# Performance work log

Hardware: AMD Instinct MI355X
Metric: run time of the kernel (lower is better)

## Reference

```python
import jax, jax.numpy as jnp
import numpy as np

N_NODES, N_FEAT, N_HID, N_CLS = 50000, 128, 64, 16
N_EDGES, N_EDGES2 = 800000, 3000000


def _rand_edges(key, n_edges, n_nodes):
    # self-loop-free random edge list [2, E] (src, dst)
    k1, k2 = jax.random.split(key)
    src = jax.random.randint(k1, (n_edges,), 0, n_nodes)
    off = jax.random.randint(k2, (n_edges,), 1, n_nodes)
    dst = (src + off) % n_nodes
    return jnp.stack([src, dst]).astype(jnp.int64)


def setup_inputs() -> dict:
    key = jax.random.key(0)
    ks = jax.random.split(key, 8)
    x = jax.random.normal(ks[0], (N_NODES, N_FEAT), jnp.float32)
    edge_index = _rand_edges(ks[1], N_EDGES, N_NODES)    # original edges, no self loops
    edge_index2 = _rand_edges(ks[2], N_EDGES2, N_NODES)  # exclusive 2-hop edges
    w1 = jax.random.normal(ks[3], (N_FEAT, N_HID), jnp.float32) / np.sqrt(N_FEAT)
    b1 = jnp.zeros((N_HID,), jnp.float32)
    w2 = jax.random.normal(ks[4], (3 * N_HID, N_CLS), jnp.float32) / np.sqrt(3 * N_HID)
    b2 = jnp.zeros((N_CLS,), jnp.float32)
    lin_w = jax.random.normal(ks[5], (3 * N_CLS, N_CLS), jnp.float32) / np.sqrt(3 * N_CLS)
    lin_b = jnp.zeros((N_CLS,), jnp.float32)
    return {"x": x, "w1": w1, "b1": b1, "w2": w2, "b2": b2,
            "lin_w": lin_w, "lin_b": lin_b,
            "edge_index": edge_index, "edge_index2": edge_index2}


def _gcn_conv(h, W, b, ei, n):
    # PyG GCNConv(add_self_loops=False): transform, symmetric-normalize, scatter-add, bias.
    hw = h @ W                                   # [n, d_out]
    src, dst = ei[0], ei[1]
    ones = jnp.ones(ei.shape[1], h.dtype)
    deg = jax.ops.segment_sum(ones, dst, num_segments=n)       # in-degree
    dinv = jnp.where(deg > 0, jax.lax.rsqrt(jnp.maximum(deg, 1e-12)), 0.0)
    norm = dinv[src] * dinv[dst]                 # [E]
    msg = hw[src] * norm[:, None]                # gather + scale (traffic-bound)
    return jax.ops.segment_sum(msg, dst, num_segments=n) + b


def reference(x, w1, b1, w2, b2, lin_w, lin_b, edge_index, edge_index2):
    n = x.shape[0]
    # layer 1: three branches over (original edges, 2-hop edges, self-loop-only)
    h1 = _gcn_conv(x, w1, b1, edge_index, n)
    h1_2 = _gcn_conv(x, w1, b1, edge_index2, n)
    h1_3 = x @ w1 + b1                           # self-loop-only GCN: deg=1, norm=1
    R1 = jax.nn.relu(jnp.concatenate([h1, h1_2, h1_3], axis=1))  # dropout = identity (eval)
    # layer 2: same three branches with shared gcn2 weights
    h2 = _gcn_conv(R1, w2, b2, edge_index, n)
    h2_2 = _gcn_conv(R1, w2, b2, edge_index2, n)
    h2_3 = R1 @ w2 + b2
    R2 = jnp.concatenate([h2, h2_2, h2_3], axis=1)
    out = R2 @ lin_w + lin_b
    return jax.nn.log_softmax(out, axis=1)
```

## Files before the change

### kernel.cpp

```cpp
#include <hip/hip_runtime.h>
#include <math.h>


#define NPB    64
#define CHUNK  16384
#define HCHUNK 16384

typedef unsigned short us8 __attribute__((ext_vector_type(8)));

__device__ inline float b2f(unsigned short u) {
    return __uint_as_float(((unsigned int)u) << 16);
}
__device__ inline unsigned short f2b(float f) {
    unsigned int u = __float_as_uint(f);
    u = (u + 0x7FFFu + ((u >> 16) & 1u)) >> 16;
    return (unsigned short)u;
}

__global__ void __launch_bounds__(256)
k_gemm1(const float* __restrict__ x, const float* __restrict__ w1,
        unsigned short* __restrict__ hwb, int n) {
    __shared__ float ws[128 * 64];
    __shared__ float xs[64 * 128];
    int t = threadIdx.x;
    int row0 = blockIdx.x * 64;
    for (int i = t; i < 128 * 16; i += 256)
        ((float4*)ws)[i] = ((const float4*)w1)[i];
    for (int i = t; i < 64 * 32; i += 256) {
        int r = row0 + (i >> 5);
        ((float4*)xs)[i] = (r < n) ? ((const float4*)x)[r * 32 + (i & 31)]
                                   : make_float4(0.f, 0.f, 0.f, 0.f);
    }
    __syncthreads();
    int tr = t >> 4, tc = t & 15;
    float acc[4][4] = {};
    #pragma unroll 4
    for (int k4 = 0; k4 < 32; ++k4) {
        float4 wv0 = *(const float4*)&ws[(k4 * 4 + 0) * 64 + tc * 4];
        float4 wv1 = *(const float4*)&ws[(k4 * 4 + 1) * 64 + tc * 4];
        float4 wv2 = *(const float4*)&ws[(k4 * 4 + 2) * 64 + tc * 4];
        float4 wv3 = *(const float4*)&ws[(k4 * 4 + 3) * 64 + tc * 4];
        #pragma unroll
        for (int r = 0; r < 4; ++r) {
            float4 xv = *(const float4*)&xs[(tr * 4 + r) * 128 + k4 * 4];
            acc[r][0] = fmaf(xv.x, wv0.x, acc[r][0]);
            acc[r][1] = fmaf(xv.x, wv0.y, acc[r][1]);
            acc[r][2] = fmaf(xv.x, wv0.z, acc[r][2]);
            acc[r][3] = fmaf(xv.x, wv0.w, acc[r][3]);
            acc[r][0] = fmaf(xv.y, wv1.x, acc[r][0]);
            acc[r][1] = fmaf(xv.y, wv1.y, acc[r][1]);
            acc[r][2] = fmaf(xv.y, wv1.z, acc[r][2]);
            acc[r][3] = fmaf(xv.y, wv1.w, acc[r][3]);
            acc[r][0] = fmaf(xv.z, wv2.x, acc[r][0]);
            acc[r][1] = fmaf(xv.z, wv2.y, acc[r][1]);
            acc[r][2] = fmaf(xv.z, wv2.z, acc[r][2]);
            acc[r][3] = fmaf(xv.z, wv2.w, acc[r][3]);
            acc[r][0] = fmaf(xv.w, wv3.x, acc[r][0]);
            acc[r][1] = fmaf(xv.w, wv3.y, acc[r][1]);
            acc[r][2] = fmaf(xv.w, wv3.z, acc[r][2]);
            acc[r][3] = fmaf(xv.w, wv3.w, acc[r][3]);
        }
    }
    #pragma unroll
    for (int r = 0; r < 4; ++r) {
        int rr = row0 + tr * 4 + r;
        if (rr < n) {
            ushort4 o;
            o.x = f2b(acc[r][0]); o.y = f2b(acc[r][1]);
            o.z = f2b(acc[r][2]); o.w = f2b(acc[r][3]);
            *(ushort4*)&hwb[rr * 64 + tc * 4] = o;
        }
    }
}

__global__ void k_hist2(const int* __restrict__ dstA, int* __restrict__ bhA, int EA, int nbA,
                        const int* __restrict__ dstB, int* __restrict__ bhB, int EB) {
    __shared__ int lh[1024];
    const int* dst; int* bh; int E; int cb;
    if ((int)blockIdx.x < nbA) { dst = dstA; bh = bhA; E = EA; cb = blockIdx.x; }
    else                       { dst = dstB; bh = bhB; E = EB; cb = blockIdx.x - nbA; }
    int t = threadIdx.x;
    for (int i = t; i < 1024; i += 256) lh[i] = 0;
    __syncthreads();
    int base = cb * HCHUNK;
    int cnt = min(HCHUNK, E - base);
    for (int i = t; i < cnt; i += 256) atomicAdd(&lh[dst[base + i] >> 6], 1);
    __syncthreads();
    for (int b = t; b < 1024; b += 256)
        if (lh[b]) atomicAdd(&bh[b], lh[b]);
}

__global__ void k_bscan(const int* __restrict__ bhA, int* __restrict__ bbA, int* __restrict__ bcA,
                        const int* __restrict__ bhB, int* __restrict__ bbB, int* __restrict__ bcB,
                        int B) {
    const int* bh = blockIdx.x ? bhB : bhA;
    int* bb = blockIdx.x ? bbB : bbA;
    int* bc = blockIdx.x ? bcB : bcA;
    int t = threadIdx.x;
    int carry = 0;
    int nch = (B + 63) >> 6;
    for (int c = 0; c < nch; ++c) {
        int idx = c * 64 + t;
        int v = (idx < B) ? bh[idx] : 0;
        int incl = v;
        #pragma unroll
        for (int off = 1; off < 64; off <<= 1) {
            int tv = __shfl_up(incl, off);
            if (t >= off) incl += tv;
        }
        if (idx < B) { bb[idx] = incl - v + carry; bc[idx] = incl - v + carry; }
        carry += __shfl(incl, 63);
    }
    if (t == 0) bb[B] = carry;
}

__global__ void __launch_bounds__(1024)
k_part2(const int* __restrict__ srcA, const int* __restrict__ dstA,
        int* __restrict__ bcurA, unsigned int* __restrict__ outA, int EA, int nbA,
        const int* __restrict__ srcB, const int* __restrict__ dstB,
        int* __restrict__ bcurB, unsigned int* __restrict__ outB, int EB) {
    __shared__ int lh[1024];
    __shared__ int loff[1024];
    __shared__ int gof[1024];
    __shared__ int lcur[1024];
    __shared__ unsigned int stage[CHUNK];
    const int *src, *dst; int *bcur; unsigned int *out; int E, cb;
    if ((int)blockIdx.x < nbA) { src = srcA; dst = dstA; bcur = bcurA; out = outA; E = EA; cb = blockIdx.x; }
    else                       { src = srcB; dst = dstB; bcur = bcurB; out = outB; E = EB; cb = blockIdx.x - nbA; }
    int t = threadIdx.x;
    int base = cb * CHUNK;
    int cnt = min(CHUNK, E - base);
    lh[t] = 0;
    __syncthreads();
    for (int i = t; i < cnt; i += 1024) atomicAdd(&lh[dst[base + i] >> 6], 1);
    __syncthreads();
    int vdeg = lh[t];
    int incl = vdeg;
    #pragma unroll
    for (int off = 1; off < 64; off <<= 1) {
        int tv = __shfl_up(incl, off);
        if ((t & 63) >= off) incl += tv;
    }
    if ((t & 63) == 63) gof[t >> 6] = incl;
    __syncthreads();
    if (t < 16) {
        int wv = gof[t];
        int winc = wv;
        #pragma unroll
        for (int off = 1; off < 16; off <<= 1) {
            int tv = __shfl_up(winc, off, 16);
            if (t >= off) winc += tv;
        }
        gof[16 + t] = winc - wv;
    }
    __syncthreads();
    int excl = incl - vdeg + gof[16 + (t >> 6)];
    loff[t] = excl;
    lcur[t] = excl;
    __syncthreads();
    gof[t] = vdeg ? atomicAdd(&bcur[t], vdeg) : 0;
    __syncthreads();
    for (int i = t; i < cnt; i += 1024) {
        int d = dst[base + i];
        int s = src[base + i];
        int bkt = d >> 6;
        int p = atomicAdd(&lcur[bkt], 1);
        stage[p] = (unsigned int)s | ((unsigned int)(d & 63) << 16) |
                   ((unsigned int)bkt << 22);
    }
    __syncthreads();
    for (int i = t; i < cnt; i += 1024) {
        unsigned int e = stage[i];
        int bkt = (int)(e >> 22);
        out[gof[bkt] + (i - loff[bkt])] = e & 0x3FFFFFu;
    }
}

__global__ void __launch_bounds__(256)
k_csr2(const int* __restrict__ bbaseA, const unsigned int* __restrict__ ebufA,
       int* __restrict__ rsA, float* __restrict__ dvA, unsigned short* __restrict__ ssrcA, int EA,
       const int* __restrict__ bbaseB, const unsigned int* __restrict__ ebufB,
       int* __restrict__ rsB, float* __restrict__ dvB, unsigned short* __restrict__ ssrcB, int EB,
       int B, int n) {
    __shared__ int cnt[64];
    __shared__ int lcur[64];
    const int* bbase; const unsigned int* ebuf; int* rs; float* dv;
    unsigned short* ssrc; int b, Etot;
    if ((int)blockIdx.x < B) { bbase = bbaseA; ebuf = ebufA; rs = rsA; dv = dvA; ssrc = ssrcA; b = blockIdx.x; Etot = EA; }
    else                     { bbase = bbaseB; ebuf = ebufB; rs = rsB; dv = dvB; ssrc = ssrcB; b = blockIdx.x - B; Etot = EB; }
    int t = threadIdx.x;
    if (t < 64) cnt[t] = 0;
    __syncthreads();
    int beg = bbase[b], end = bbase[b + 1];
    for (int i = beg + t; i < end; i += 256)
        atomicAdd(&cnt[(ebuf[i] >> 16) & 63u], 1);
    __syncthreads();
    if (t < 64) {
        int v = cnt[t];
        int incl = v;
        #pragma unroll
        for (int off = 1; off < 64; off <<= 1) {
            int tv = __shfl_up(incl, off);
            if (t >= off) incl += tv;
        }
        int start = beg + incl - v;
        lcur[t] = start;
        int node = b * NPB + t;
        if (node < n) {
            rs[node] = start;
            dv[node] = (v > 0) ? rsqrtf((float)v) : 0.f;
        }
    }
    __syncthreads();
    for (int i = beg + t; i < end; i += 256) {
        unsigned int e = ebuf[i];
        int p = atomicAdd(&lcur[(e >> 16) & 63u], 1);
        ssrc[p] = (unsigned short)(e & 0xFFFFu);
    }
    if (t == 0 && b == B - 1) rs[n] = Etot;
}

__global__ void k_pack(const unsigned short* __restrict__ ssrc1, const float* __restrict__ dinv1,
                       unsigned int* __restrict__ p1, int E1,
                       const unsigned short* __restrict__ ssrc2, const float* __restrict__ dinv2,
                       unsigned int* __restrict__ p2, int E2) {
    int stride = gridDim.x * 256;
    for (int i = blockIdx.x * 256 + threadIdx.x; i < E1 + E2; i += stride) {
        if (i < E1) {
            int s = ssrc1[i];
            p1[i] = (unsigned int)s | ((unsigned int)f2b(dinv1[s]) << 16);
        } else {
            int j = i - E1;
            int s = ssrc2[j];
            p2[j] = (unsigned int)s | ((unsigned int)f2b(dinv2[s]) << 16);
        }
    }
}

__device__ inline void agg64_body(const int* __restrict__ rs,
                                  const unsigned int* __restrict__ psrc,
                                  const float* __restrict__ dinv,
                                  const us8* __restrict__ hwb8,
                                  const float* __restrict__ b1,
                                  unsigned short* __restrict__ R1b,
                                  int col_unit, int n, int tid) {
    int v = tid >> 3, q = tid & 7;
    if (v >= n) return;
    int beg = rs[v], end = rs[v + 1];
    float a[8] = {0.f, 0.f, 0.f, 0.f, 0.f, 0.f, 0.f, 0.f};
    int i = beg;
    for (; i + 8 <= end; i += 8) {
        unsigned int e0 = psrc[i + 0], e1 = psrc[i + 1], e2 = psrc[i + 2], e3 = psrc[i + 3];
        unsigned int e4 = psrc[i + 4], e5 = psrc[i + 5], e6 = psrc[i + 6], e7 = psrc[i + 7];
        int s0 = e0 & 0xFFFFu, s1 = e1 & 0xFFFFu, s2 = e2 & 0xFFFFu, s3 = e3 & 0xFFFFu;
        int s4 = e4 & 0xFFFFu, s5 = e5 & 0xFFFFu, s6 = e6 & 0xFFFFu, s7 = e7 & 0xFFFFu;
        float c0 = b2f((unsigned short)(e0 >> 16)), c1 = b2f((unsigned short)(e1 >> 16));
        float c2 = b2f((unsigned short)(e2 >> 16)), c3 = b2f((unsigned short)(e3 >> 16));
        float c4 = b2f((unsigned short)(e4 >> 16)), c5 = b2f((unsigned short)(e5 >> 16));
        float c6 = b2f((unsigned short)(e6 >> 16)), c7 = b2f((unsigned short)(e7 >> 16));
        us8 h0 = hwb8[s0 * 8 + q], h1 = hwb8[s1 * 8 + q];
        us8 h2 = hwb8[s2 * 8 + q], h3 = hwb8[s3 * 8 + q];
        us8 h4 = hwb8[s4 * 8 + q], h5 = hwb8[s5 * 8 + q];
        us8 h6 = hwb8[s6 * 8 + q], h7 = hwb8[s7 * 8 + q];
        #pragma unroll
        for (int j = 0; j < 8; ++j) {
            a[j] = fmaf(b2f(h0[j]), c0, a[j]);
            a[j] = fmaf(b2f(h1[j]), c1, a[j]);
            a[j] = fmaf(b2f(h2[j]), c2, a[j]);
            a[j] = fmaf(b2f(h3[j]), c3, a[j]);
            a[j] = fmaf(b2f(h4[j]), c4, a[j]);
            a[j] = fmaf(b2f(h5[j]), c5, a[j]);
            a[j] = fmaf(b2f(h6[j]), c6, a[j]);
            a[j] = fmaf(b2f(h7[j]), c7, a[j]);
        }
    }
    for (; i < end; ++i) {
        unsigned int e = psrc[i];
        int s = e & 0xFFFFu;
        float sc = b2f((unsigned short)(e >> 16));
        us8 h = hwb8[s * 8 + q];
        #pragma unroll
        for (int j = 0; j < 8; ++j) a[j] = fmaf(b2f(h[j]), sc, a[j]);
    }
    float dd = dinv[v];
    us8 o;
    #pragma unroll
    for (int j = 0; j < 8; ++j) {
        float r = fmaf(a[j], dd, b1[q * 8 + j]);
        o[j] = f2b(r > 0.f ? r : 0.f);
    }
    ((us8*)&R1b[v * 192])[col_unit + q] = o;
}

__global__ void k_agg1f(const int* __restrict__ rs1, const unsigned int* __restrict__ psrc1,
                        const float* __restrict__ dinv1,
                        const int* __restrict__ rs2, const unsigned int* __restrict__ psrc2,
                        const float* __restrict__ dinv2,
                        const us8* __restrict__ hwb8, const float* __restrict__ b1,
                        unsigned short* __restrict__ R1b, int n, int nba) {
    int bid = blockIdx.x;
    if (bid < nba) {
        agg64_body(rs2, psrc2, dinv2, hwb8, b1, R1b, 8, n, bid * 256 + threadIdx.x);
    } else if (bid < 2 * nba) {
        agg64_body(rs1, psrc1, dinv1, hwb8, b1, R1b, 0, n,
                   (bid - nba) * 256 + threadIdx.x);
    } else {
        int tid = (bid - 2 * nba) * 256 + threadIdx.x;
        int v = tid >> 3, q = tid & 7;
        if (v >= n) return;
        us8 h = hwb8[v * 8 + q];
        us8 o;
        #pragma unroll
        for (int j = 0; j < 8; ++j) {
            float r = b2f(h[j]) + b1[q * 8 + j];
            o[j] = f2b(r > 0.f ? r : 0.f);
        }
        ((us8*)&R1b[v * 192])[16 + q] = o;
    }
}

__global__ void __launch_bounds__(256)
k_gemm2(const unsigned short* __restrict__ R1b, const float* __restrict__ w2,
        unsigned short* __restrict__ hwb2, int n) {
    __shared__ float ws[192 * 16];
    __shared__ float rs[16][193];
    int t = threadIdx.x;
    for (int i = t; i < 192 * 16; i += 256) ws[i] = w2[i];
    int row0 = blockIdx.x * 16;
    for (int i = t; i < 16 * 192; i += 256) {
        int r = i / 192, j = i - r * 192;
        int v = row0 + r;
        rs[r][j] = (v < n) ? b2f(R1b[v * 192 + j]) : 0.f;
    }
    __syncthreads();
    int r = t >> 4, c = t & 15;
    int v = row0 + r;
    if (v >= n) return;
    float acc = 0.f;
    #pragma unroll 8
    for (int j = 0; j < 192; ++j) acc += rs[r][j] * ws[j * 16 + c];
    hwb2[v * 16 + c] = f2b(acc);
}

__device__ inline void gath16(const int* __restrict__ rs,
                              const unsigned int* __restrict__ psrc,
                              const us8* __restrict__ h8,
                              int v, int q, float* __restrict__ a) {
    int beg = rs[v], end = rs[v + 1];
    #pragma unroll
    for (int j = 0; j < 8; ++j) a[j] = 0.f;
    int i = beg;
    for (; i + 8 <= end; i += 8) {
        unsigned int e0 = psrc[i + 0], e1 = psrc[i + 1], e2 = psrc[i + 2], e3 = psrc[i + 3];
        unsigned int e4 = psrc[i + 4], e5 = psrc[i + 5], e6 = psrc[i + 6], e7 = psrc[i + 7];
        int s0 = e0 & 0xFFFFu, s1 = e1 & 0xFFFFu, s2 = e2 & 0xFFFFu, s3 = e3 & 0xFFFFu;
        int s4 = e4 & 0xFFFFu, s5 = e5 & 0xFFFFu, s6 = e6 & 0xFFFFu, s7 = e7 & 0xFFFFu;
        float c0 = b2f((unsigned short)(e0 >> 16)), c1 = b2f((unsigned short)(e1 >> 16));
        float c2 = b2f((unsigned short)(e2 >> 16)), c3 = b2f((unsigned short)(e3 >> 16));
        float c4 = b2f((unsigned short)(e4 >> 16)), c5 = b2f((unsigned short)(e5 >> 16));
        float c6 = b2f((unsigned short)(e6 >> 16)), c7 = b2f((unsigned short)(e7 >> 16));
        us8 h0 = h8[s0 * 2 + q], h1 = h8[s1 * 2 + q];
        us8 h2 = h8[s2 * 2 + q], h3 = h8[s3 * 2 + q];
        us8 h4 = h8[s4 * 2 + q], h5 = h8[s5 * 2 + q];
        us8 h6 = h8[s6 * 2 + q], h7 = h8[s7 * 2 + q];
        #pragma unroll
        for (int j = 0; j < 8; ++j) {
            a[j] = fmaf(b2f(h0[j]), c0, a[j]);
            a[j] = fmaf(b2f(h1[j]), c1, a[j]);
            a[j] = fmaf(b2f(h2[j]), c2, a[j]);
            a[j] = fmaf(b2f(h3[j]), c3, a[j]);
            a[j] = fmaf(b2f(h4[j]), c4, a[j]);
            a[j] = fmaf(b2f(h5[j]), c5, a[j]);
            a[j] = fmaf(b2f(h6[j]), c6, a[j]);
            a[j] = fmaf(b2f(h7[j]), c7, a[j]);
        }
    }
    for (; i < end; ++i) {
        unsigned int e = psrc[i];
        int s = e & 0xFFFFu;
        float sc = b2f((unsigned short)(e >> 16));
        us8 h = h8[s * 2 + q];
        #pragma unroll
        for (int j = 0; j < 8; ++j) a[j] = fmaf(b2f(h[j]), sc, a[j]);
    }
}

__global__ void __launch_bounds__(256)
k_l2f(const int* __restrict__ rs1, const unsigned int* __restrict__ psrc1,
      const float* __restrict__ dinv1,
      const int* __restrict__ rs2, const unsigned int* __restrict__ psrc2,
      const float* __restrict__ dinv2,
      const us8* __restrict__ hwb2_8, const unsigned short* __restrict__ hwb2,
      const float* __restrict__ b2, const float* __restrict__ lw,
      const float* __restrict__ lb, float* __restrict__ out, int n) {
    __shared__ float accA[128 * 16];
    __shared__ float accB[128 * 16];
    __shared__ float lws[48 * 16];
    __shared__ float r2s[16][49];
    int t = threadIdx.x;
    int v0 = blockIdx.x * 128;
    for (int i = t; i < 48 * 16; i += 256) lws[i] = lw[i];
    int vl = t >> 1, q = t & 1;
    int v = v0 + vl;
    if (v < n) {
        float a[8];
        gath16(rs2, psrc2, hwb2_8, v, q, a);
        #pragma unroll
        for (int j = 0; j < 8; ++j) accB[vl * 16 + q * 8 + j] = a[j];
        gath16(rs1, psrc1, hwb2_8, v, q, a);
        #pragma unroll
        for (int j = 0; j < 8; ++j) accA[vl * 16 + q * 8 + j] = a[j];
    }
    __syncthreads();
    int ni = t >> 4, c = t & 15;
    for (int p = 0; p < 8; ++p) {
        int vv = v0 + p * 16 + ni;
        int vl2 = p * 16 + ni;
        if (vv < n) {
            float bb = b2[c];
            r2s[ni][c]      = fmaf(dinv1[vv], accA[vl2 * 16 + c], bb);
            r2s[ni][16 + c] = fmaf(dinv2[vv], accB[vl2 * 16 + c], bb);
            r2s[ni][32 + c] = b2f(hwb2[vv * 16 + c]) + bb;
        }
        __syncthreads();
        if (vv < n) {
            float o = lb[c];
            #pragma unroll
            for (int j = 0; j < 48; ++j) o += r2s[ni][j] * lws[j * 16 + c];
            float m = o;
            for (int off = 8; off >= 1; off >>= 1) m = fmaxf(m, __shfl_xor(m, off, 16));
            float e = expf(o - m);
            float ssum = e;
            for (int off = 8; off >= 1; off >>= 1) ssum += __shfl_xor(ssum, off, 16);
            out[vv * 16 + c] = (o - m) - logf(ssum);
        }
        __syncthreads();
    }
}

extern "C" void kernel_launch(void* const* d_in, const int* in_sizes, int n_in,
                              void* d_out, int out_size, void* d_ws, size_t ws_size,
                              hipStream_t stream) {
    const float* x     = (const float*)d_in[0];
    const float* w1    = (const float*)d_in[1];
    const float* b1    = (const float*)d_in[2];
    const float* w2    = (const float*)d_in[3];
    const float* b2    = (const float*)d_in[4];
    const float* lin_w = (const float*)d_in[5];
    const float* lin_b = (const float*)d_in[6];
    const int*   ei    = (const int*)d_in[7];
    const int*   ei2   = (const int*)d_in[8];

    const int n  = in_sizes[0] / 128;
    const int E1 = in_sizes[7] / 2;
    const int E2 = in_sizes[8] / 2;
    const int B  = (n + NPB - 1) / NPB;

    char* ws = (char*)d_ws;
    unsigned short* hwb   = (unsigned short*)(ws + 0);
    unsigned short* hwb2  = (unsigned short*)(ws + 6400000);
    unsigned short* R1b   = (unsigned short*)(ws + 8000000);
    unsigned short* ssrc1 = (unsigned short*)(ws + 27200000);
    unsigned short* ssrc2 = (unsigned short*)(ws + 28800000);
    unsigned int* ebuf1   = (unsigned int*)(ws + 34800000);
    unsigned int* ebuf2   = (unsigned int*)(ws + 38000000);
    unsigned int* psrc1   = ebuf1;
    unsigned int* psrc2   = ebuf2;
    float*        dinv1   = (float*)(ws + 56800000);
    float*        dinv2   = (float*)(ws + 57000000);
    int*          rs1     = (int*)(ws + 57200000);
    int*          rs2     = (int*)(ws + 57400016);
    int*          bhist1  = (int*)(ws + 58000032);
    int*          bhist2  = (int*)(ws + 58004128);
    int*          bbase1  = (int*)(ws + 58008224);
    int*          bbase2  = (int*)(ws + 58012320);
    int*          bcur1   = (int*)(ws + 58016416);
    int*          bcur2   = (int*)(ws + 58020512);

    hipMemsetAsync(bhist1, 0, 8192, stream);

    k_gemm1<<<(n + 63) / 64, 256, 0, stream>>>(x, w1, hwb, n);

    const int nbh1 = (E1 + HCHUNK - 1) / HCHUNK, nbh2 = (E2 + HCHUNK - 1) / HCHUNK;
    k_hist2<<<nbh1 + nbh2, 256, 0, stream>>>(ei + E1, bhist1, E1, nbh1,
                                             ei2 + E2, bhist2, E2);
    k_bscan<<<2, 64, 0, stream>>>(bhist1, bbase1, bcur1, bhist2, bbase2, bcur2, B);

    const int nbp1 = (E1 + CHUNK - 1) / CHUNK, nbp2 = (E2 + CHUNK - 1) / CHUNK;
    k_part2<<<nbp1 + nbp2, 1024, 0, stream>>>(ei, ei + E1, bcur1, ebuf1, E1, nbp1,
                                              ei2, ei2 + E2, bcur2, ebuf2, E2);

    k_csr2<<<2 * B, 256, 0, stream>>>(bbase1, ebuf1, rs1, dinv1, ssrc1, E1,
                                      bbase2, ebuf2, rs2, dinv2, ssrc2, E2, B, n);

    k_pack<<<2048, 256, 0, stream>>>(ssrc1, dinv1, psrc1, E1, ssrc2, dinv2, psrc2, E2);

    const int nba = (n * 8 + 255) / 256;
    k_agg1f<<<3 * nba, 256, 0, stream>>>(rs1, psrc1, dinv1, rs2, psrc2, dinv2,
                                         (const us8*)hwb, b1, R1b, n, nba);

    k_gemm2<<<(n + 15) / 16, 256, 0, stream>>>(R1b, w2, hwb2, n);

    k_l2f<<<(n + 127) / 128, 256, 0, stream>>>(rs1, psrc1, dinv1, rs2, psrc2, dinv2,
                                               (const us8*)hwb2, hwb2, b2,
                                               lin_w, lin_b, (float*)d_out, n);
}
```

Measured before the change: 244.2 us.

## Scatter partition directly to global and fuse agg1 branches per node

The partition kernel no longer stages edges in a 64KB shared buffer with a local prefix scan. Each edge now takes a per-bucket slot through a shared atomic counter and is written straight to its global position. This frees a large amount of LDS, which should raise occupancy, and removes the scan and a barrier, at the cost of less coalesced global writes. The layer-1 aggregation kernel now handles both edge sets and the self-loop branch in one thread per node slice instead of three separate block ranges. That launches fewer blocks and shares the row addressing, but serialises the work per thread.

```diff
diff --git a/kernel.cpp b/kernel.cpp
--- a/kernel.cpp
+++ b/kernel.cpp
@@ -120,10 +120,8 @@
         const int* __restrict__ srcB, const int* __restrict__ dstB,
         int* __restrict__ bcurB, unsigned int* __restrict__ outB, int EB) {
     __shared__ int lh[1024];
-    __shared__ int loff[1024];
     __shared__ int gof[1024];
     __shared__ int lcur[1024];
-    __shared__ unsigned int stage[CHUNK];
     const int *src, *dst; int *bcur; unsigned int *out; int E, cb;
     if ((int)blockIdx.x < nbA) { src = srcA; dst = dstA; bcur = bcurA; out = outA; E = EA; cb = blockIdx.x; }
     else                       { src = srcB; dst = dstB; bcur = bcurB; out = outB; E = EB; cb = blockIdx.x - nbA; }
@@ -131,48 +129,18 @@
     int base = cb * CHUNK;
     int cnt = min(CHUNK, E - base);
     lh[t] = 0;
+    lcur[t] = 0;
     __syncthreads();
     for (int i = t; i < cnt; i += 1024) atomicAdd(&lh[dst[base + i] >> 6], 1);
     __syncthreads();
-    int vdeg = lh[t];
-    int incl = vdeg;
-    #pragma unroll
-    for (int off = 1; off < 64; off <<= 1) {
-        int tv = __shfl_up(incl, off);
-        if ((t & 63) >= off) incl += tv;
-    }
-    if ((t & 63) == 63) gof[t >> 6] = incl;
-    __syncthreads();
-    if (t < 16) {
-        int wv = gof[t];
-        int winc = wv;
-        #pragma unroll
-        for (int off = 1; off < 16; off <<= 1) {
-            int tv = __shfl_up(winc, off, 16);
-            if (t >= off) winc += tv;
-        }
-        gof[16 + t] = winc - wv;
-    }
-    __syncthreads();
-    int excl = incl - vdeg + gof[16 + (t >> 6)];
-    loff[t] = excl;
-    lcur[t] = excl;
-    __syncthreads();
-    gof[t] = vdeg ? atomicAdd(&bcur[t], vdeg) : 0;
+    gof[t] = lh[t] ? atomicAdd(&bcur[t], lh[t]) : 0;
     __syncthreads();
     for (int i = t; i < cnt; i += 1024) {
         int d = dst[base + i];
         int s = src[base + i];
         int bkt = d >> 6;
         int p = atomicAdd(&lcur[bkt], 1);
-        stage[p] = (unsigned int)s | ((unsigned int)(d & 63) << 16) |
-                   ((unsigned int)bkt << 22);
-    }
-    __syncthreads();
-    for (int i = t; i < cnt; i += 1024) {
-        unsigned int e = stage[i];
-        int bkt = (int)(e >> 22);
-        out[gof[bkt] + (i - loff[bkt])] = e & 0x3FFFFFu;
+        out[gof[bkt] + p] = (unsigned int)s | ((unsigned int)(d & 63) << 16);
     }
 }
 
@@ -237,17 +205,12 @@
     }
 }
 
-__device__ inline void agg64_body(const int* __restrict__ rs,
-                                  const unsigned int* __restrict__ psrc,
-                                  const float* __restrict__ dinv,
-                                  const us8* __restrict__ hwb8,
-                                  const float* __restrict__ b1,
-                                  unsigned short* __restrict__ R1b,
-                                  int col_unit, int n, int tid) {
-    int v = tid >> 3, q = tid & 7;
-    if (v >= n) return;
-    int beg = rs[v], end = rs[v + 1];
-    float a[8] = {0.f, 0.f, 0.f, 0.f, 0.f, 0.f, 0.f, 0.f};
+__device__ inline void agg64_acc(int beg, int end,
+                                 const unsigned int* __restrict__ psrc,
+                                 const us8* __restrict__ hwb8, int q,
+                                 float* __restrict__ a) {
+    #pragma unroll
+    for (int j = 0; j < 8; ++j) a[j] = 0.f;
     int i = beg;
     for (; i + 8 <= end; i += 8) {
         unsigned int e0 = psrc[i + 0], e1 = psrc[i + 1], e2 = psrc[i + 2], e3 = psrc[i + 3];
@@ -282,14 +245,6 @@
         #pragma unroll
         for (int j = 0; j < 8; ++j) a[j] = fmaf(b2f(h[j]), sc, a[j]);
     }
-    float dd = dinv[v];
-    us8 o;
-    #pragma unroll
-    for (int j = 0; j < 8; ++j) {
-        float r = fmaf(a[j], dd, b1[q * 8 + j]);
-        o[j] = f2b(r > 0.f ? r : 0.f);
-    }
-    ((us8*)&R1b[v * 192])[col_unit + q] = o;
 }
 
 __global__ void k_agg1f(const int* __restrict__ rs1, const unsigned int* __restrict__ psrc1,
@@ -297,26 +252,36 @@
                         const int* __restrict__ rs2, const unsigned int* __restrict__ psrc2,
                         const float* __restrict__ dinv2,
                         const us8* __restrict__ hwb8, const float* __restrict__ b1,
-                        unsigned short* __restrict__ R1b, int n, int nba) {
-    int bid = blockIdx.x;
-    if (bid < nba) {
-        agg64_body(rs2, psrc2, dinv2, hwb8, b1, R1b, 8, n, bid * 256 + threadIdx.x);
-    } else if (bid < 2 * nba) {
-        agg64_body(rs1, psrc1, dinv1, hwb8, b1, R1b, 0, n,
-                   (bid - nba) * 256 + threadIdx.x);
-    } else {
-        int tid = (bid - 2 * nba) * 256 + threadIdx.x;
-        int v = tid >> 3, q = tid & 7;
-        if (v >= n) return;
-        us8 h = hwb8[v * 8 + q];
-        us8 o;
-        #pragma unroll
-        for (int j = 0; j < 8; ++j) {
-            float r = b2f(h[j]) + b1[q * 8 + j];
-            o[j] = f2b(r > 0.f ? r : 0.f);
-        }
-        ((us8*)&R1b[v * 192])[16 + q] = o;
-    }
+                        unsigned short* __restrict__ R1b, int n) {
+    int tid = blockIdx.x * 256 + threadIdx.x;
+    int v = tid >> 3, q = tid & 7;
+    if (v >= n) return;
+    float a[8];
+    us8* rowOut = (us8*)&R1b[v * 192];
+    agg64_acc(rs2[v], rs2[v + 1], psrc2, hwb8, q, a);
+    float dd2 = dinv2[v];
+    us8 o;
+    #pragma unroll
+    for (int j = 0; j < 8; ++j) {
+        float r = fmaf(a[j], dd2, b1[q * 8 + j]);
+        o[j] = f2b(r > 0.f ? r : 0.f);
+    }
+    rowOut[8 + q] = o;
+    agg64_acc(rs1[v], rs1[v + 1], psrc1, hwb8, q, a);
+    float dd1 = dinv1[v];
+    #pragma unroll
+    for (int j = 0; j < 8; ++j) {
+        float r = fmaf(a[j], dd1, b1[q * 8 + j]);
+        o[j] = f2b(r > 0.f ? r : 0.f);
+    }
+    rowOut[q] = o;
+    us8 h = hwb8[v * 8 + q];
+    #pragma unroll
+    for (int j = 0; j < 8; ++j) {
+        float r = b2f(h[j]) + b1[q * 8 + j];
+        o[j] = f2b(r > 0.f ? r : 0.f);
+    }
+    rowOut[16 + q] = o;
 }
 
 __global__ void __launch_bounds__(256)
@@ -495,9 +460,9 @@
 
     k_pack<<<2048, 256, 0, stream>>>(ssrc1, dinv1, psrc1, E1, ssrc2, dinv2, psrc2, E2);
 
-    const int nba = (n * 8 + 255) / 256;
-    k_agg1f<<<3 * nba, 256, 0, stream>>>(rs1, psrc1, dinv1, rs2, psrc2, dinv2,
-                                         (const us8*)hwb, b1, R1b, n, nba);
+    k_agg1f<<<(n * 8 + 255) / 256, 256, 0, stream>>>(rs1, psrc1, dinv1,
+                                                     rs2, psrc2, dinv2,
+                                                     (const us8*)hwb, b1, R1b, n);
 
     k_gemm2<<<(n + 15) / 16, 256, 0, stream>>>(R1b, w2, hwb2, n);
 
```

Result: slower. 265.7 us (+8.8%).
